# Performance work log

Hardware: AMD Instinct MI355X
Metric: run time of the kernel (lower is better)

The kernel has to match this reference:

```python
import jax, jax.numpy as jnp
import numpy as np

WS = 4           # window_size
NUM_HEADS = 4
LN_EPS = 1e-5


def setup_inputs() -> dict:
    key = jax.random.key(0)
    ks = jax.random.split(key, 8)
    d = 256
    s = 0.02
    return {
        "feature": jax.random.normal(ks[0], (8, d, 127, 127), dtype=jnp.float32),
        "ln_w": jnp.ones((d,), jnp.float32),
        "ln_b": jnp.zeros((d,), jnp.float32),
        "in_w": jax.random.normal(ks[1], (3 * d, d), jnp.float32) * s,
        "in_b": jnp.zeros((3 * d,), jnp.float32),
        "out_w": jax.random.normal(ks[2], (d, d), jnp.float32) * s,
        "out_b": jnp.zeros((d,), jnp.float32),
        "proj_w": jax.random.normal(ks[3], (d, d), jnp.float32) * s,
        "proj_b": jnp.zeros((d,), jnp.float32),
    }


def reference(feature, ln_w, ln_b, in_w, in_b, out_w, out_b, proj_w, proj_b):
    B, C, H, W = feature.shape
    ws = WS
    pad_h = (-H) % ws
    pad_w = (-W) % ws
    x = jnp.pad(feature, ((0, 0), (0, 0), (0, pad_h), (0, pad_w)))
    Hp, Wp = H + pad_h, W + pad_w
    nh, nw = Hp // ws, Wp // ws
    # NCHW -> NHWC -> windows [B*nh*nw, ws*ws, C]
    x = x.transpose(0, 2, 3, 1)
    win = (x.reshape(B, nh, ws, nw, ws, C)
            .transpose(0, 1, 3, 2, 4, 5)
            .reshape(-1, ws * ws, C))
    # LayerNorm (ddof=0, matches torch)
    mu = win.mean(-1, keepdims=True)
    var = win.var(-1, keepdims=True)
    xn = (win - mu) / jnp.sqrt(var + LN_EPS) * ln_w + ln_b
    # fused QKV projection, then split heads
    qkv = xn @ in_w.T + in_b
    q, k, v = jnp.split(qkv, 3, axis=-1)
    hd = C // NUM_HEADS
    def heads(t):
        return t.reshape(t.shape[0], t.shape[1], NUM_HEADS, hd).transpose(0, 2, 1, 3)
    q, k, v = heads(q), heads(k), heads(v)
    scores = jnp.einsum('bhqd,bhkd->bhqk', q, k) / np.float32(np.sqrt(hd))
    a = jax.nn.softmax(scores, axis=-1)
    o = jnp.einsum('bhqk,bhkd->bhqd', a, v)
    o = o.transpose(0, 2, 1, 3).reshape(-1, ws * ws, C)
    o = o @ out_w.T + out_b
    # residual + Linear + exact GELU
    y = win + jax.nn.gelu(o @ proj_w.T + proj_b, approximate=False)
    # windows -> NHWC, crop padding, -> NCHW
    y = (y.reshape(B, nh, nw, ws, ws, C)
          .transpose(0, 1, 3, 2, 4, 5)
          .reshape(B, Hp, Wp, C))
    return y[:, :H, :W, :].transpose(0, 3, 1, 2)
```

## Files before the change

kernel.cpp:

```cpp
#include <hip/hip_runtime.h>

typedef _Float16 f16;
typedef __attribute__((ext_vector_type(4))) _Float16 half4;
typedef __attribute__((ext_vector_type(8))) _Float16 half8;
typedef __attribute__((ext_vector_type(4))) float f32x4;
typedef unsigned short u16;

#define MFMA32(a,b,c) __builtin_amdgcn_mfma_f32_16x16x32_f16(a,b,c,0,0,0)
#define MFMA16(a,b,c) __builtin_amdgcn_mfma_f32_16x16x16f16(a,b,c,0,0,0)

#define W_IN0   0
#define W_OUT0  196608
#define W_PROJ0 262144
#define X0      327680
#define QK0     33882112ull
#define VT0     100990976ull

__global__ void k0_cast(const float* __restrict__ iw, const float* __restrict__ ow,
                        const float* __restrict__ pw, f16* __restrict__ W) {
    int i = blockIdx.x * 256 + threadIdx.x;
    if (i < 196608) W[W_IN0 + i] = (f16)iw[i];
    if (i < 65536) {
        W[W_OUT0 + i]  = (f16)ow[i];
        W[W_PROJ0 + i] = (f16)pw[i];
    }
}

__global__ __launch_bounds__(256, 4)
void k1_pack(const float* __restrict__ feat, const float* __restrict__ lnw,
             const float* __restrict__ lnb, f16* __restrict__ X) {
    const int tid = threadIdx.x, lane = tid & 63, hh = tid >> 6;
    const int bid = blockIdx.x;
    const int jh = bid & 3, wi = (bid >> 2) & 31, bb = bid >> 7;
    const int h0 = wi * 4, w0 = jh * 32;
    const int wl4 = lane & 7, cg = lane >> 3;
    const int h = h0 + hh, wb = w0 + wl4 * 4;
    const bool hok = (h < 127);
    const bool edge = (wb + 3) >= 127;
    const size_t bbase = (size_t)bb * (256 * 127 * 127);
    const int c0 = cg * 32;
    const float* p0 = feat + bbase + (size_t)c0 * 16129 + (size_t)h * 127 + wb;

    half4 arr[32];
    float ss[4] = {0.f, 0.f, 0.f, 0.f}, qq[4] = {0.f, 0.f, 0.f, 0.f};
    if (hok && !edge) {
#pragma unroll
        for (int i = 0; i < 32; ++i) {
            f32x4 v = *(const f32x4*)(p0 + (size_t)i * 16129);
            half4 hv;
#pragma unroll
            for (int e = 0; e < 4; ++e) { ss[e] += v[e]; qq[e] += v[e] * v[e]; hv[e] = (f16)v[e]; }
            arr[i] = hv;
        }
    } else if (hok) {
#pragma unroll
        for (int i = 0; i < 32; ++i) {
            const float* pi = p0 + (size_t)i * 16129;
            half4 hv;
#pragma unroll
            for (int e = 0; e < 3; ++e) { float v = pi[e]; ss[e] += v; qq[e] += v * v; hv[e] = (f16)v; }
            hv[3] = (f16)0.f;
            arr[i] = hv;
        }
    } else {
#pragma unroll
        for (int i = 0; i < 32; ++i) {
            half4 hv; hv[0] = hv[1] = hv[2] = hv[3] = (f16)0.f; arr[i] = hv;
        }
    }
#pragma unroll
    for (int e = 0; e < 4; ++e) {
        ss[e] += __shfl_xor(ss[e], 8);  qq[e] += __shfl_xor(qq[e], 8);
        ss[e] += __shfl_xor(ss[e], 16); qq[e] += __shfl_xor(qq[e], 16);
        ss[e] += __shfl_xor(ss[e], 32); qq[e] += __shfl_xor(qq[e], 32);
    }
    float mu[4], rs[4];
#pragma unroll
    for (int e = 0; e < 4; ++e) {
        mu[e] = ss[e] * (1.f / 256.f);
        rs[e] = rsqrtf(qq[e] * (1.f / 256.f) - mu[e] * mu[e] + 1e-5f);
    }
#pragma unroll
    for (int q = 0; q < 4; ++q) {
        f32x4 lw0 = *(const f32x4*)(lnw + c0 + q * 8);
        f32x4 lw1 = *(const f32x4*)(lnw + c0 + q * 8 + 4);
        f32x4 lb0 = *(const f32x4*)(lnb + c0 + q * 8);
        f32x4 lb1 = *(const f32x4*)(lnb + c0 + q * 8 + 4);
#pragma unroll
        for (int e = 0; e < 4; ++e) {
            const int m = wl4 * 16 + hh * 4 + e;
            f16* xrow = X + ((size_t)bid * 128 + m) * 256 + c0;
            half8 o;
#pragma unroll
            for (int j = 0; j < 4; ++j) {
                o[j]     = (f16)(((float)arr[q * 8 + j][e]     - mu[e]) * rs[e] * lw0[j] + lb0[j]);
                o[j + 4] = (f16)(((float)arr[q * 8 + j + 4][e] - mu[e]) * rs[e] * lw1[j] + lb1[j]);
            }
            *(half8*)(xrow + q * 8) = o;
        }
    }
}

__global__ __launch_bounds__(256, 2)
void k2_qkv(const f16* __restrict__ X, const f16* __restrict__ win,
            const float* __restrict__ inb, f16* __restrict__ QK, f16* __restrict__ VT) {
    __shared__ __align__(16) char sm[65536];
    const int tid = threadIdx.x, lane = tid & 63, wv = tid >> 6;
    const int nwg = gridDim.x;
    const int bid = (blockIdx.x & 7) * (nwg >> 3) + (blockIdx.x >> 3);
    const int mt = bid / 6, nb = bid % 6;
    const size_t Mbase = (size_t)mt * 128;
    const int n0 = nb * 128;
    const int wm = wv >> 1, wn = wv & 1;
    const int c = lane & 15, g = lane >> 4;
    const int r8 = lane >> 3, chv = lane & 7;

    f32x4 acc[4][4];
#pragma unroll
    for (int a = 0; a < 4; ++a)
#pragma unroll
        for (int b = 0; b < 4; ++b) acc[a][b] = f32x4{0.f, 0.f, 0.f, 0.f};

    auto stage = [&](int step, int bsel) {
        const f16* As = X + Mbase * 256 + step * 64;
        const f16* Bs = win + (size_t)n0 * 256 + step * 64;
#pragma unroll
        for (int q = 0; q < 4; ++q) {
            int ia = wv * 4 + q;
            int row = ia * 8 + r8;
            int chs = chv ^ (row & 7);
            __builtin_amdgcn_global_load_lds(
                (const __attribute__((address_space(1))) unsigned int*)(As + (size_t)row * 256 + chs * 8),
                (__attribute__((address_space(3))) unsigned int*)(sm + bsel * 32768 + ia * 1024),
                16, 0, 0);
            __builtin_amdgcn_global_load_lds(
                (const __attribute__((address_space(1))) unsigned int*)(Bs + (size_t)row * 256 + chs * 8),
                (__attribute__((address_space(3))) unsigned int*)(sm + bsel * 32768 + 16384 + ia * 1024),
                16, 0, 0);
        }
    };
    stage(0, 0);
    __syncthreads();
    for (int s = 0; s < 4; ++s) {
        int bsel = s & 1;
        if (s < 3) stage(s + 1, bsel ^ 1);
#pragma unroll
        for (int kk2 = 0; kk2 < 2; ++kk2) {
            half8 a[4], b[4];
#pragma unroll
            for (int mi = 0; mi < 4; ++mi) {
                int row = wm * 64 + mi * 16 + c;
                a[mi] = *(half8*)(sm + bsel * 32768 + row * 128 + ((kk2 * 64 + g * 16) ^ ((row & 7) << 4)));
            }
#pragma unroll
            for (int nt = 0; nt < 4; ++nt) {
                int row = wn * 64 + nt * 16 + c;
                b[nt] = *(half8*)(sm + bsel * 32768 + 16384 + row * 128 + ((kk2 * 64 + g * 16) ^ ((row & 7) << 4)));
            }
#pragma unroll
            for (int mi = 0; mi < 4; ++mi)
#pragma unroll
                for (int nt = 0; nt < 4; ++nt)
                    acc[mi][nt] = MFMA32(a[mi], b[nt], acc[mi][nt]);
        }
        __syncthreads();
    }

    const f32x4 z4 = {0.f, 0.f, 0.f, 0.f};
    half4 idf;
#pragma unroll
    for (int j = 0; j < 4; ++j) idf[j] = (f16)((g * 4 + j == c) ? 1.f : 0.f);

    if (n0 < 512) {
#pragma unroll
        for (int mi = 0; mi < 4; ++mi)
#pragma unroll
            for (int nt = 0; nt < 4; ++nt) {
                int n = n0 + wn * 64 + nt * 16 + c;
                float bias = inb[n];
                half4 h;
#pragma unroll
                for (int r = 0; r < 4; ++r) h[r] = (f16)(acc[mi][nt][r] + bias);
                f32x4 t = MFMA16(h, idf, z4);
                half4 o;
#pragma unroll
                for (int r = 0; r < 4; ++r) o[r] = (f16)t[r];
                size_t tok = Mbase + wm * 64 + mi * 16 + c;
                *(half4*)(QK + tok * 512 + (n0 + wn * 64 + nt * 16 + g * 4)) = o;
            }
    } else {
#pragma unroll
        for (int mi = 0; mi < 4; ++mi)
#pragma unroll
            for (int nt = 0; nt < 4; ++nt) {
                int n = n0 + wn * 64 + nt * 16 + c;
                float bias = inb[n];
                half4 h;
#pragma unroll
                for (int r = 0; r < 4; ++r) h[r] = (f16)(acc[mi][nt][r] + bias);
                int d = n - 512;
                size_t tokb = Mbase + wm * 64 + mi * 16;
                size_t winI = tokb >> 4;
                *(half4*)(VT + winI * 4096 + (size_t)d * 16 + g * 4) = h;
            }
    }
}

__global__ __launch_bounds__(256, 3)
void k3_attn(const f16* __restrict__ QK, const f16* __restrict__ VT,
             const f16* __restrict__ wout, const f16* __restrict__ wproj,
             const float* __restrict__ outb, const float* __restrict__ projb,
             f16* __restrict__ G) {
    __shared__ __align__(16) char sm[32768];
    const int tid = threadIdx.x, lane = tid & 63, wv = tid >> 6;
    const int c = lane & 15, g = lane >> 4;
    const size_t win = (size_t)blockIdx.x * 4 + wv;
    const f16* qrow = QK + (win * 16 + c) * 512;
    const f32x4 z4 = {0.f, 0.f, 0.f, 0.f};

    const int nl = tid >> 3, seg = tid & 7;
    const int swz = (nl & 15) << 3;
    auto stageW = [&](const f16* mat, int rc, int bsel) {
        const f16* src = mat + ((size_t)(rc * 32 + nl)) * 256 + seg * 32;
        char* dst = sm + bsel * 16384 + nl * 512;
#pragma unroll
        for (int i = 0; i < 4; ++i) {
            uint4 u = *(const uint4*)(src + i * 8);
            int b0 = (seg * 64 + i * 16) ^ swz;
            int b1 = (seg * 64 + i * 16 + 8) ^ swz;
            *(uint2*)(dst + b0) = make_uint2(u.x, u.y);
            *(uint2*)(dst + b1) = make_uint2(u.z, u.w);
        }
    };

    stageW(wout, 0, 0);

    half4 of16[4][4];
#pragma unroll
    for (int hq = 0; hq < 4; ++hq) {
        half8 af0 = *(const half8*)(qrow + 256 + hq * 64 + g * 8);
        half8 af1 = *(const half8*)(qrow + 256 + hq * 64 + 32 + g * 8);
        half8 bq0 = *(const half8*)(qrow + hq * 64 + g * 8);
        half8 bq1 = *(const half8*)(qrow + hq * 64 + 32 + g * 8);
        f32x4 sacc = MFMA32(af0, bq0, z4);
        sacc = MFMA32(af1, bq1, sacc);
        float s0 = sacc[0] * 0.125f, s1 = sacc[1] * 0.125f;
        float s2 = sacc[2] * 0.125f, s3 = sacc[3] * 0.125f;
        float mx = fmaxf(fmaxf(s0, s1), fmaxf(s2, s3));
        mx = fmaxf(mx, __shfl_xor(mx, 16));
        mx = fmaxf(mx, __shfl_xor(mx, 32));
        float p0 = __expf(s0 - mx), p1 = __expf(s1 - mx);
        float p2 = __expf(s2 - mx), p3 = __expf(s3 - mx);
        float sum = p0 + p1 + p2 + p3;
        sum += __shfl_xor(sum, 16);
        sum += __shfl_xor(sum, 32);
        float inv = 1.f / sum;
        half4 pf;
        pf[0] = (f16)(p0 * inv); pf[1] = (f16)(p1 * inv);
        pf[2] = (f16)(p2 * inv); pf[3] = (f16)(p3 * inv);
#pragma unroll
        for (int nt = 0; nt < 4; ++nt) {
            half4 vf = *(const half4*)(VT + win * 4096 + (size_t)(hq * 64 + nt * 16 + c) * 16 + g * 4);
            f32x4 o = MFMA16(vf, pf, z4);
            half4 oh;
#pragma unroll
            for (int r = 0; r < 4; ++r) oh[r] = (f16)o[r];
            of16[hq][nt] = oh;
        }
    }

    f32x4 obacc[16];
#pragma unroll
    for (int i = 0; i < 16; ++i) obacc[i] = z4;
    __syncthreads();
#pragma unroll
    for (int ch = 0; ch < 8; ++ch) {
        if (ch < 7) stageW(wout, ch + 1, (ch + 1) & 1);
        else        stageW(wproj, 0, (ch + 1) & 1);
        int bsel = ch & 1;
#pragma unroll
        for (int ntl = 0; ntl < 2; ++ntl) {
            int nt2 = ch * 2 + ntl;
            int rowl = ntl * 16 + c;
            char* base = sm + bsel * 16384 + rowl * 512;
            int sw2 = (rowl & 15) << 3;
            f32x4 a = obacc[nt2];
#pragma unroll
            for (int hq = 0; hq < 4; ++hq)
#pragma unroll
                for (int dt = 0; dt < 4; ++dt) {
                    half4 wf = *(const half4*)(base + (((hq * 64 + dt * 16 + g * 4) * 2) ^ sw2));
                    a = MFMA16(wf, of16[hq][dt], a);
                }
            obacc[nt2] = a;
        }
        __syncthreads();
    }
    half4 obT[16];
#pragma unroll
    for (int nt = 0; nt < 16; ++nt) {
        f32x4 bv = *(const f32x4*)(outb + nt * 16 + g * 4);
        half4 h;
#pragma unroll
        for (int r = 0; r < 4; ++r) h[r] = (f16)(obacc[nt][r] + bv[r]);
        obT[nt] = h;
    }

    f32x4 yacc[16];
#pragma unroll
    for (int i = 0; i < 16; ++i) yacc[i] = z4;
#pragma unroll
    for (int pc = 0; pc < 8; ++pc) {
        if (pc < 7) stageW(wproj, pc + 1, (pc + 1) & 1);
        int bsel = pc & 1;
#pragma unroll
        for (int ntl = 0; ntl < 2; ++ntl) {
            int nt3 = pc * 2 + ntl;
            int rowl = ntl * 16 + c;
            char* base = sm + bsel * 16384 + rowl * 512;
            int sw2 = (rowl & 15) << 3;
            f32x4 a = yacc[nt3];
#pragma unroll
            for (int ntc = 0; ntc < 16; ++ntc) {
                half4 wf = *(const half4*)(base + (((ntc * 16 + g * 4) * 2) ^ sw2));
                a = MFMA16(wf, obT[ntc], a);
            }
            yacc[nt3] = a;
        }
        __syncthreads();
    }

#pragma unroll
    for (int nt = 0; nt < 16; ++nt) {
        f32x4 bv = *(const f32x4*)(projb + nt * 16 + g * 4);
        half4 h;
#pragma unroll
        for (int r = 0; r < 4; ++r) {
            float x = yacc[nt][r] + bv[r];
            h[r] = (f16)(0.5f * x * (1.f + erff(x * 0.70710678118f)));
        }
        *(half4*)(G + (win * 16 + c) * 256 + nt * 16 + g * 4) = h;
    }
}

__global__ __launch_bounds__(256, 8)
void k4_out(const f16* __restrict__ G, const float* __restrict__ feat, float* __restrict__ outp) {
    const int tid = threadIdx.x;
    const int bid = blockIdx.x;
    const int bb = bid / 127, h = bid % 127;
    const int w = tid & 127;
    const int cq = tid >> 7;
    const bool wok = (w < 127);
    const size_t bbase = (size_t)bb * (256 * 127 * 127);
    const int wi = h >> 2, hh = h & 3;
    const int jh = w >> 5, wl4 = (w >> 2) & 7, e = w & 3;
    const size_t t = ((size_t)((bb * 32 + wi) * 4 + jh)) * 128 + wl4 * 16 + hh * 4 + e;
    const f16* gp = G + t * 256;
    const float* fp = feat + bbase + (size_t)h * 127 + w;
    float* op = outp + bbase + (size_t)h * 127 + w;
#pragma unroll 4
    for (int ci = 0; ci < 32; ++ci) {
        const int ch = ci * 8 + cq * 4;
        if (wok) {
            half4 g4 = *(const half4*)(gp + ch);
#pragma unroll
            for (int j = 0; j < 4; ++j) {
                size_t off = (size_t)(ch + j) * 16129;
                op[off] = fp[off] + (float)g4[j];
            }
        }
    }
}

extern "C" void kernel_launch(void* const* d_in, const int* in_sizes, int n_in,
                              void* d_out, int out_size, void* d_ws, size_t ws_size,
                              hipStream_t stream) {
    const float* feat   = (const float*)d_in[0];
    const float* ln_w   = (const float*)d_in[1];
    const float* ln_b   = (const float*)d_in[2];
    const float* in_w   = (const float*)d_in[3];
    const float* in_b   = (const float*)d_in[4];
    const float* out_w  = (const float*)d_in[5];
    const float* out_b  = (const float*)d_in[6];
    const float* proj_w = (const float*)d_in[7];
    const float* proj_b = (const float*)d_in[8];

    f16* W  = (f16*)d_ws;
    f16* Xb  = W + X0;
    f16* QKb = W + QK0;
    f16* VTb = W + VT0;
    f16* Gb  = Xb;

    k0_cast<<<768, 256, 0, stream>>>(in_w, out_w, proj_w, W);
    k1_pack<<<1024, 256, 0, stream>>>(feat, ln_w, ln_b, Xb);
    k2_qkv<<<6144, 256, 0, stream>>>(Xb, W + W_IN0, in_b, QKb, VTb);
    k3_attn<<<2048, 256, 0, stream>>>(QKb, VTb, W + W_OUT0, W + W_PROJ0, out_b, proj_b, Gb);
    k4_out<<<1016, 256, 0, stream>>>(Gb, feat, (float*)d_out);
}
```

Measured before the change: 386.6 us.

## Pre-swizzle out/proj weights and stream them to LDS via global_load_lds with 16x16x32 MFMAs

The cast kernel now writes the out and proj weight matrices in a pre-swizzled, chunked layout, so the attention kernel can copy them straight into LDS with global_load_lds. This replaces the register round trip and manual swizzled stores. The two post-attention GEMMs switch from 16x16x16 to 16x16x32 MFMAs with half8 operands, halving the MFMA instruction count. The out-projection result is converted to fp16 per chunk rather than kept in sixteen fp32 accumulators, which reduces register pressure. The final barrier is skipped on the last chunk. This relies on the packed k-order of the attention outputs matching the swizzled weight layout.

```diff
diff --git a/kernel.cpp b/kernel.cpp
--- a/kernel.cpp
+++ b/kernel.cpp
@@ -20,9 +20,20 @@
                         const float* __restrict__ pw, f16* __restrict__ W) {
     int i = blockIdx.x * 256 + threadIdx.x;
     if (i < 196608) W[W_IN0 + i] = (f16)iw[i];
-    if (i < 65536) {
-        W[W_OUT0 + i]  = (f16)ow[i];
-        W[W_PROJ0 + i] = (f16)pw[i];
+    if (i < 16384) {
+        const int s = i & 8191;
+        const float* src = (i < 8192) ? ow : pw;
+        f16* dst = W + ((i < 8192) ? W_OUT0 : W_PROJ0);
+        const int r = s >> 5, sp = s & 31;
+        const int u = sp ^ (r & 7);
+        const int kc = u >> 2, gg = u & 3;
+        const int c0 = kc * 32 + gg * 4;
+        f32x4 v0 = *(const f32x4*)(src + r * 256 + c0);
+        f32x4 v1 = *(const f32x4*)(src + r * 256 + c0 + 16);
+        half8 o;
+#pragma unroll
+        for (int j = 0; j < 4; ++j) { o[j] = (f16)v0[j]; o[j + 4] = (f16)v1[j]; }
+        *(half8*)(dst + (r >> 5) * 8192 + (r & 31) * 256 + sp * 8) = o;
     }
 }
 
@@ -218,24 +229,20 @@
     const f16* qrow = QK + (win * 16 + c) * 512;
     const f32x4 z4 = {0.f, 0.f, 0.f, 0.f};
 
-    const int nl = tid >> 3, seg = tid & 7;
-    const int swz = (nl & 15) << 3;
-    auto stageW = [&](const f16* mat, int rc, int bsel) {
-        const f16* src = mat + ((size_t)(rc * 32 + nl)) * 256 + seg * 32;
-        char* dst = sm + bsel * 16384 + nl * 512;
-#pragma unroll
-        for (int i = 0; i < 4; ++i) {
-            uint4 u = *(const uint4*)(src + i * 8);
-            int b0 = (seg * 64 + i * 16) ^ swz;
-            int b1 = (seg * 64 + i * 16 + 8) ^ swz;
-            *(uint2*)(dst + b0) = make_uint2(u.x, u.y);
-            *(uint2*)(dst + b1) = make_uint2(u.z, u.w);
+    auto stageW = [&](const f16* img, int rc, int bsel) {
+#pragma unroll
+        for (int q2 = 0; q2 < 4; ++q2) {
+            int ia = wv * 4 + q2;
+            __builtin_amdgcn_global_load_lds(
+                (const __attribute__((address_space(1))) unsigned int*)(img + rc * 8192 + ia * 512 + lane * 8),
+                (__attribute__((address_space(3))) unsigned int*)(sm + bsel * 16384 + ia * 1024),
+                16, 0, 0);
         }
     };
 
     stageW(wout, 0, 0);
 
-    half4 of16[4][4];
+    half8 ofp[4][2];
 #pragma unroll
     for (int hq = 0; hq < 4; ++hq) {
         half8 af0 = *(const half8*)(qrow + 256 + hq * 64 + g * 8);
@@ -262,84 +269,65 @@
         for (int nt = 0; nt < 4; ++nt) {
             half4 vf = *(const half4*)(VT + win * 4096 + (size_t)(hq * 64 + nt * 16 + c) * 16 + g * 4);
             f32x4 o = MFMA16(vf, pf, z4);
-            half4 oh;
-#pragma unroll
-            for (int r = 0; r < 4; ++r) oh[r] = (f16)o[r];
-            of16[hq][nt] = oh;
-        }
-    }
-
-    f32x4 obacc[16];
-#pragma unroll
-    for (int i = 0; i < 16; ++i) obacc[i] = z4;
+#pragma unroll
+            for (int r = 0; r < 4; ++r) ofp[hq][nt >> 1][(nt & 1) * 4 + r] = (f16)o[r];
+        }
+    }
+
+    const int r0 = c, r1 = 16 + c;
+    const int sw0 = (r0 & 7) << 4, sw1 = (r1 & 7) << 4;
+    half8 obp[8];
     __syncthreads();
+
 #pragma unroll
     for (int ch = 0; ch < 8; ++ch) {
         if (ch < 7) stageW(wout, ch + 1, (ch + 1) & 1);
         else        stageW(wproj, 0, (ch + 1) & 1);
-        int bsel = ch & 1;
-#pragma unroll
-        for (int ntl = 0; ntl < 2; ++ntl) {
-            int nt2 = ch * 2 + ntl;
-            int rowl = ntl * 16 + c;
-            char* base = sm + bsel * 16384 + rowl * 512;
-            int sw2 = (rowl & 15) << 3;
-            f32x4 a = obacc[nt2];
-#pragma unroll
-            for (int hq = 0; hq < 4; ++hq)
-#pragma unroll
-                for (int dt = 0; dt < 4; ++dt) {
-                    half4 wf = *(const half4*)(base + (((hq * 64 + dt * 16 + g * 4) * 2) ^ sw2));
-                    a = MFMA16(wf, of16[hq][dt], a);
-                }
-            obacc[nt2] = a;
+        char* base = sm + (ch & 1) * 16384;
+        f32x4 a0 = z4, a1 = z4;
+#pragma unroll
+        for (int kc = 0; kc < 8; ++kc) {
+            half8 w0 = *(half8*)(base + r0 * 512 + ((kc * 64 + g * 16) ^ sw0));
+            a0 = MFMA32(w0, ofp[kc >> 1][kc & 1], a0);
+            half8 w1 = *(half8*)(base + r1 * 512 + ((kc * 64 + g * 16) ^ sw1));
+            a1 = MFMA32(w1, ofp[kc >> 1][kc & 1], a1);
+        }
+        f32x4 b0 = *(const f32x4*)(outb + ch * 32 + g * 4);
+        f32x4 b1 = *(const f32x4*)(outb + ch * 32 + 16 + g * 4);
+#pragma unroll
+        for (int r = 0; r < 4; ++r) {
+            obp[ch][r]     = (f16)(a0[r] + b0[r]);
+            obp[ch][4 + r] = (f16)(a1[r] + b1[r]);
         }
         __syncthreads();
     }
-    half4 obT[16];
-#pragma unroll
-    for (int nt = 0; nt < 16; ++nt) {
-        f32x4 bv = *(const f32x4*)(outb + nt * 16 + g * 4);
-        half4 h;
-#pragma unroll
-        for (int r = 0; r < 4; ++r) h[r] = (f16)(obacc[nt][r] + bv[r]);
-        obT[nt] = h;
-    }
-
-    f32x4 yacc[16];
-#pragma unroll
-    for (int i = 0; i < 16; ++i) yacc[i] = z4;
+
 #pragma unroll
     for (int pc = 0; pc < 8; ++pc) {
         if (pc < 7) stageW(wproj, pc + 1, (pc + 1) & 1);
-        int bsel = pc & 1;
-#pragma unroll
-        for (int ntl = 0; ntl < 2; ++ntl) {
-            int nt3 = pc * 2 + ntl;
-            int rowl = ntl * 16 + c;
-            char* base = sm + bsel * 16384 + rowl * 512;
-            int sw2 = (rowl & 15) << 3;
-            f32x4 a = yacc[nt3];
-#pragma unroll
-            for (int ntc = 0; ntc < 16; ++ntc) {
-                half4 wf = *(const half4*)(base + (((ntc * 16 + g * 4) * 2) ^ sw2));
-                a = MFMA16(wf, obT[ntc], a);
-            }
-            yacc[nt3] = a;
-        }
-        __syncthreads();
-    }
-
-#pragma unroll
-    for (int nt = 0; nt < 16; ++nt) {
-        f32x4 bv = *(const f32x4*)(projb + nt * 16 + g * 4);
-        half4 h;
+        char* base = sm + (pc & 1) * 16384;
+        f32x4 a0 = z4, a1 = z4;
+#pragma unroll
+        for (int kc = 0; kc < 8; ++kc) {
+            half8 w0 = *(half8*)(base + r0 * 512 + ((kc * 64 + g * 16) ^ sw0));
+            a0 = MFMA32(w0, obp[kc], a0);
+            half8 w1 = *(half8*)(base + r1 * 512 + ((kc * 64 + g * 16) ^ sw1));
+            a1 = MFMA32(w1, obp[kc], a1);
+        }
+        f32x4 b0 = *(const f32x4*)(projb + pc * 32 + g * 4);
+        f32x4 b1 = *(const f32x4*)(projb + pc * 32 + 16 + g * 4);
+        half4 h0, h1;
 #pragma unroll
         for (int r = 0; r < 4; ++r) {
-            float x = yacc[nt][r] + bv[r];
-            h[r] = (f16)(0.5f * x * (1.f + erff(x * 0.70710678118f)));
-        }
-        *(half4*)(G + (win * 16 + c) * 256 + nt * 16 + g * 4) = h;
+            float x0 = a0[r] + b0[r];
+            h0[r] = (f16)(0.5f * x0 * (1.f + erff(x0 * 0.70710678118f)));
+            float x1 = a1[r] + b1[r];
+            h1[r] = (f16)(0.5f * x1 * (1.f + erff(x1 * 0.70710678118f)));
+        }
+        f16* grow = G + (win * 16 + c) * 256 + pc * 32;
+        *(half4*)(grow + g * 4) = h0;
+        *(half4*)(grow + 16 + g * 4) = h1;
+        if (pc < 7) __syncthreads();
     }
 }
 
```

Result: faster. 367.0 us (-5.1%).
